# Optimization experiments

Measured on AMD Instinct MI355X. Metric: run time of the kernel, lower is better.

Reference implementation:

```python
import jax, jax.numpy as jnp
import numpy as np

BS, NC, BH, BW, C = 1, 6, 100, 100, 256
HG, WG = 100, 40
HF, WF = 48, 80
HEADS, PTS, HD = 8, 8, 32
MAXOV = 2
NQ = HG * WG


def _nearest_sample(img, grid):
    # img: [B,H,W,Ch], grid: [B,Hg,Wg,2] in [-1,1]; nearest, align_corners=True, zeros padding
    B, H, W, _ = img.shape
    ix = jnp.round((grid[..., 0] + 1.0) * 0.5 * (W - 1))
    iy = jnp.round((grid[..., 1] + 1.0) * 0.5 * (H - 1))
    valid = (ix >= 0) & (ix <= W - 1) & (iy >= 0) & (iy <= H - 1)
    xc = jnp.clip(ix, 0, W - 1).astype(jnp.int32)
    yc = jnp.clip(iy, 0, H - 1).astype(jnp.int32)
    b = jnp.arange(B)[:, None, None]
    return img[b, yc, xc] * valid[..., None]


def _bilinear_sample(img, x, y):
    # img: [B,H,W,Ch]; x,y: [B,N] unnormalized (align_corners=False); zeros padding
    B, H, W, _ = img.shape
    x0 = jnp.floor(x)
    y0 = jnp.floor(y)
    wx1 = x - x0
    wy1 = y - y0
    b = jnp.arange(B)[:, None]

    def corner(xi, yi):
        valid = (xi >= 0) & (xi <= W - 1) & (yi >= 0) & (yi <= H - 1)
        xc = jnp.clip(xi, 0, W - 1).astype(jnp.int32)
        yc = jnp.clip(yi, 0, H - 1).astype(jnp.int32)
        return img[b, yc, xc] * valid[..., None]

    return (corner(x0, y0) * ((1 - wx1) * (1 - wy1))[..., None]
            + corner(x0 + 1, y0) * (wx1 * (1 - wy1))[..., None]
            + corner(x0, y0 + 1) * ((1 - wx1) * wy1)[..., None]
            + corner(x0 + 1, y0 + 1) * (wx1 * wy1)[..., None])


def _forward(query, value, queries_rebatch_grid, restore_bev_grid,
             reference_points_rebatch, bev_pillar_counts, query_pos,
             Wv, bv, Woff, boff, Watt, batt, Wout, bout, spatial_shapes):
    inp_residual = query
    q = query + query_pos                                       # [BS, BH*BW, C]
    # --- rebatch BEV queries per camera via nearest grid_sample ---
    qmap = jnp.broadcast_to(q.reshape(BS, 1, BH, BW, C),
                            (BS, NC, BH, BW, C)).reshape(BS * NC, BH, BW, C)
    q_reb = _nearest_sample(qmap, queries_rebatch_grid).reshape(BS * NC, NQ, C)
    ref = reference_points_rebatch.reshape(BS * NC, NQ, 2)      # flatten(-2): [BNC,NQ,2,1]->[BNC,NQ,2]
    # --- value projection ---
    v = value.transpose(2, 0, 1, 3).reshape(BS * NC, HF * WF, C)
    v = (v @ Wv + bv).reshape(BS * NC, HF, WF, HEADS, HD)
    # --- multi-scale deformable attention (single level) ---
    off = (q_reb @ Woff + boff).reshape(BS * NC, NQ, HEADS, PTS, 2)
    attw = jax.nn.softmax((q_reb @ Watt + batt).reshape(BS * NC, NQ, HEADS, PTS), axis=-1)
    normalizer = jnp.flip(spatial_shapes[0], 0).astype(jnp.float32)  # [WF, HF]
    loc = ref[:, :, None, None, :] + off / normalizer           # [BNC,NQ,HEADS,PTS,2] in [0,1]
    x = (loc[..., 0] * WF - 0.5).transpose(0, 2, 1, 3).reshape(BS * NC * HEADS, NQ * PTS)
    y = (loc[..., 1] * HF - 0.5).transpose(0, 2, 1, 3).reshape(BS * NC * HEADS, NQ * PTS)
    vh = v.transpose(0, 3, 1, 2, 4).reshape(BS * NC * HEADS, HF, WF, HD)
    samp = _bilinear_sample(vh, x, y).reshape(BS * NC, HEADS, NQ, PTS, HD)
    out = jnp.einsum('bhnpd,bnhp->bnhd', samp, attw).reshape(BS * NC, NQ, C)
    queries_out = out.transpose(0, 2, 1)                        # [BNC, C, NQ] (channels-first as module expects)
    # --- restore to BEV feature ---
    qo = queries_out.reshape(BS, NC, C, NQ).transpose(0, 2, 1, 3).reshape(BS, C, NC * HG, WG)
    bevq = _nearest_sample(qo.transpose(0, 2, 3, 1), restore_bev_grid)  # [BS, MAXOV*BH, BW, C]
    bevq = bevq.transpose(0, 3, 1, 2)                           # [BS, C, MAXOV*BH, BW]
    # reshape(BS, C*MAXOV, BH, BW) + all-ones grouped 1x1 conv == sum of the two overlap copies
    slots = bevq[:, :, :BH, :] + bevq[:, :, BH:, :]             # [BS, C, BH, BW]
    slots = slots.reshape(BS, C, BH * BW).transpose(0, 2, 1)    # [BS, BH*BW, C]
    slots = slots * bev_pillar_counts
    slots = slots @ Wout + bout
    return slots + inp_residual  # dropout identity in eval


def setup_inputs():
    key = jax.random.key(0)
    ks = jax.random.split(key, 14)
    s = 1.0 / np.sqrt(C)
    return {
        "query": jax.random.normal(ks[0], (BS, BH * BW, C), jnp.float32),
        "value": jax.random.normal(ks[1], (BS, HF * WF, NC, C), jnp.float32),
        "queries_rebatch_grid": jax.random.uniform(ks[2], (BS * NC, HG, WG, 2), jnp.float32, -1.0, 1.0),
        "restore_bev_grid": jax.random.uniform(ks[3], (BS, MAXOV * BH, BW, 2), jnp.float32, -1.0, 1.0),
        "reference_points_rebatch": jax.random.uniform(ks[4], (BS * NC, NQ, 2, 1), jnp.float32),
        "bev_pillar_counts": jax.random.uniform(ks[5], (BS, BH * BW, 1), jnp.float32),
        "query_pos": jax.random.normal(ks[6], (BS, BH * BW, C), jnp.float32),
        "Wv": jax.random.uniform(ks[7], (C, C), jnp.float32, -s, s),
        "bv": jnp.zeros((C,), jnp.float32),
        "Woff": jax.random.normal(ks[8], (C, HEADS * PTS * 2), jnp.float32) * 0.01,
        "boff": jax.random.uniform(ks[9], (HEADS * PTS * 2,), jnp.float32, -2.0, 2.0),
        "Watt": jax.random.normal(ks[10], (C, HEADS * PTS), jnp.float32) * 0.01,
        "batt": jnp.zeros((HEADS * PTS,), jnp.float32),
        "Wout": jax.random.uniform(ks[11], (C, C), jnp.float32, -s, s),
        "bout": jnp.zeros((C,), jnp.float32),
        "spatial_shapes": jnp.array([[HF, WF]], dtype=jnp.int32),
    }


def reference(query, value, queries_rebatch_grid, restore_bev_grid,
              reference_points_rebatch, bev_pillar_counts, query_pos,
              Wv, bv, Woff, boff, Watt, batt, Wout, bout, spatial_shapes):
    return _forward(query, value, queries_rebatch_grid, restore_bev_grid,
                    reference_points_rebatch, bev_pillar_counts, query_pos,
                    Wv, bv, Woff, boff, Watt, batt, Wout, bout, spatial_shapes)
```

## Files before the change

### kernel.cpp

```cpp
#include <hip/hip_runtime.h>
#include <hip/hip_bf16.h>
#include <math.h>

#define NCAMS 6
#define BH_ 100
#define BW_ 100
#define CDIM 256
#define NQ_ 4000
#define HF_ 48
#define WF_ 80
#define HEADS_ 8
#define PTS_ 8
#define HD_ 32
#define HWV (HF_*WF_)
#define M1_ (NCAMS*HWV)
#define M2_ (NCAMS*NQ_)
#define NOUT_ 10000

#define SA 264
#define SOFF 132
#define SATT 68

typedef __bf16 bf16_t;
typedef __bf16 bf16x8 __attribute__((ext_vector_type(8)));
typedef __bf16 bf16x4 __attribute__((ext_vector_type(4)));
typedef float  f32x4  __attribute__((ext_vector_type(4)));

static __device__ __forceinline__ f32x4 mfma16(bf16x8 a, bf16x8 b, f32x4 c) {
    return __builtin_amdgcn_mfma_f32_16x16x32_bf16(a, b, c, 0, 0, 0);
}

__global__ __launch_bounds__(256) void k0_prep(const float* __restrict__ Wv,
                                               const float* __restrict__ Woff,
                                               const float* __restrict__ Watt,
                                               const float* __restrict__ Wout,
                                               const float* __restrict__ query,
                                               const float* __restrict__ qpos,
                                               bf16_t* __restrict__ WvT,
                                               bf16_t* __restrict__ WcombT,
                                               bf16_t* __restrict__ WoutT,
                                               bf16_t* __restrict__ qsum) {
    int b = blockIdx.x, k = threadIdx.x;
    if (b < 256) {
        WvT[b * 256 + k] = (bf16_t)Wv[k * 256 + b];
    } else if (b < 448) {
        int n = b - 256;
        float v = (n < 128) ? Woff[k * 128 + n] : Watt[k * 64 + (n - 128)];
        WcombT[n * 256 + k] = (bf16_t)v;
    } else if (b < 704) {
        int n = b - 448;
        WoutT[n * 256 + k] = (bf16_t)Wout[k * 256 + n];
    } else {
        int row0 = (b - 704) * 4;
        int r = k >> 6, c4 = k & 63;
        int i = (row0 + r) * 64 + c4;
        float4 a = ((const float4*)query)[i];
        float4 p = ((const float4*)qpos)[i];
        bf16x4 pk;
        pk[0] = (bf16_t)(a.x + p.x); pk[1] = (bf16_t)(a.y + p.y);
        pk[2] = (bf16_t)(a.z + p.z); pk[3] = (bf16_t)(a.w + p.w);
        *(bf16x4*)(qsum + (size_t)i * 4) = pk;
    }
}

__global__ __launch_bounds__(256) void k1_vproj(const float* __restrict__ value,
                                                const bf16_t* __restrict__ WvT,
                                                const float* __restrict__ bv,
                                                bf16_t* __restrict__ vh) {
    __shared__ __align__(16) bf16_t At[32 * SA];
    const int m0 = blockIdx.x * 32;
    const int cam = m0 / HWV;
    const int hw0 = m0 - cam * HWV;
    for (int idx = threadIdx.x; idx < 32 * 64; idx += 256) {
        int r = idx >> 6, c4 = idx & 63;
        float4 v = ((const float4*)value)[((hw0 + r) * NCAMS + cam) * 64 + c4];
        bf16x4 pk; pk[0] = (bf16_t)v.x; pk[1] = (bf16_t)v.y; pk[2] = (bf16_t)v.z; pk[3] = (bf16_t)v.w;
        *(bf16x4*)(At + r * SA + c4 * 4) = pk;
    }
    __syncthreads();
    const int lane = threadIdx.x & 63, w = threadIdx.x >> 6;
    const int lr = lane & 15, lk = lane >> 4;
    f32x4 acc[2][4] = {};
    const bf16_t* a0 = At + lr * SA + lk * 8;
    const bf16_t* b0 = WvT + (w * 64 + lr) * 256 + lk * 8;
#pragma unroll
    for (int ks = 0; ks < 8; ++ks) {
        bf16x8 af[2], bf_[4];
#pragma unroll
        for (int mm = 0; mm < 2; ++mm) af[mm] = *(const bf16x8*)(a0 + mm * 16 * SA + ks * 32);
#pragma unroll
        for (int n = 0; n < 4; ++n) bf_[n] = *(const bf16x8*)(b0 + n * 16 * 256 + ks * 32);
#pragma unroll
        for (int mm = 0; mm < 2; ++mm)
#pragma unroll
            for (int n = 0; n < 4; ++n)
                acc[mm][n] = mfma16(af[mm], bf_[n], acc[mm][n]);
    }
    __syncthreads();
#pragma unroll
    for (int n = 0; n < 4; ++n) {
        int col = w * 64 + n * 16 + lr;
        float bias = bv[col];
#pragma unroll
        for (int mm = 0; mm < 2; ++mm)
#pragma unroll
            for (int j = 0; j < 4; ++j)
                At[(mm * 16 + lk * 4 + j) * SA + col] = (bf16_t)(acc[mm][n][j] + bias);
    }
    __syncthreads();
    for (int idx = threadIdx.x; idx < 32 * 32; idx += 256) {
        int r = idx >> 5, g = idx & 31;
        int head = g >> 2, part = g & 3;
        bf16x8 v = *(const bf16x8*)(At + r * SA + g * 8);
        *(bf16x8*)(vh + ((size_t)(cam * HEADS_ + head) * HWV + hw0 + r) * HD_ + part * 8) = v;
    }
}

__global__ __launch_bounds__(256) void k23_offatt_sample(
        const bf16_t* __restrict__ qsum,
        const float* __restrict__ qgrid,
        const bf16_t* __restrict__ WcombT,
        const float* __restrict__ boff,
        const float* __restrict__ batt,
        const float* __restrict__ refp,
        const bf16_t* __restrict__ vh,
        bf16_t* __restrict__ out_attn) {
    __shared__ __align__(16) char u_lds[16 * SOFF * 4 + 16 * SATT * 4];
    bf16_t* At   = (bf16_t*)u_lds;
    float*  offs = (float*)u_lds;
    float*  atts = (float*)(u_lds + 16 * SOFF * 4);
    __shared__ int rowpos[16];
    __shared__ float rref[16][2];

    const int orig = blockIdx.x;
    const int xcd = orig & 7, idx8 = orig >> 3;
    const int lb = (xcd < 4 ? xcd * 188 : 4 * 188 + (xcd - 4) * 187) + idx8;
    const int m0 = lb * 16;
    const int cam = m0 / NQ_;

    if (threadIdx.x < 16) {
        int m = m0 + threadIdx.x;
        float gx = qgrid[m * 2 + 0], gy = qgrid[m * 2 + 1];
        float fx = rintf(__fmul_rn(__fmul_rn(__fadd_rn(gx, 1.0f), 0.5f), 99.0f));
        float fy = rintf(__fmul_rn(__fmul_rn(__fadd_rn(gy, 1.0f), 0.5f), 99.0f));
        bool valid = (fx >= 0.0f) && (fx <= 99.0f) && (fy >= 0.0f) && (fy <= 99.0f);
        rowpos[threadIdx.x] = valid ? ((int)fy * BW_ + (int)fx) : -1;
    } else if (threadIdx.x < 48) {
        int t = threadIdx.x - 16;
        rref[t >> 1][t & 1] = refp[(m0 + (t >> 1)) * 2 + (t & 1)];
    }
    __syncthreads();
    {
        int idx = threadIdx.x;
#pragma unroll
        for (int it = 0; it < 2; ++it, idx += 256) {
            int r = idx >> 5, g = idx & 31;
            int p = rowpos[r];
            bf16x8 v;
            if (p >= 0) v = *(const bf16x8*)(qsum + (size_t)p * 256 + g * 8);
            else { bf16x8 z = {}; v = z; }
            *(bf16x8*)(At + r * SA + g * 8) = v;
        }
    }
    __syncthreads();
    const int lane = threadIdx.x & 63, w = threadIdx.x >> 6;
    const int lr = lane & 15, lk = lane >> 4;
    const int wcol0 = w * 48;
    f32x4 acc[3] = {};
    {
        const bf16_t* a0 = At + lr * SA + lk * 8;
        const bf16_t* b0 = WcombT + (wcol0 + lr) * 256 + lk * 8;
#pragma unroll
        for (int ks = 0; ks < 8; ++ks) {
            bf16x8 af = *(const bf16x8*)(a0 + ks * 32);
            bf16x8 bf_[3];
#pragma unroll
            for (int n = 0; n < 3; ++n) bf_[n] = *(const bf16x8*)(b0 + n * 16 * 256 + ks * 32);
#pragma unroll
            for (int n = 0; n < 3; ++n)
                acc[n] = mfma16(af, bf_[n], acc[n]);
        }
    }
    __syncthreads();
#pragma unroll
    for (int n = 0; n < 3; ++n) {
        const int colbase = wcol0 + n * 16;
        const int col = colbase + lr;
        const int rloc = lk * 4;
        if (colbase < 128) {
            float bo = boff[col];
#pragma unroll
            for (int j = 0; j < 4; ++j)
                offs[(rloc + j) * SOFF + col] = acc[n][j] + bo;
        } else {
            float bt = batt[col - 128];
#pragma unroll
            for (int j = 0; j < 4; ++j) {
                float lg = acc[n][j] + bt;
                float mx = lg;
                mx = fmaxf(mx, __shfl_xor(mx, 1, 64));
                mx = fmaxf(mx, __shfl_xor(mx, 2, 64));
                mx = fmaxf(mx, __shfl_xor(mx, 4, 64));
                float e = expf(lg - mx);
                float s = e;
                s += __shfl_xor(s, 1, 64);
                s += __shfl_xor(s, 2, 64);
                s += __shfl_xor(s, 4, 64);
                atts[(rloc + j) * SATT + (col - 128)] = e / s;
            }
        }
    }
    __syncthreads();
    const int j = threadIdx.x & 3;
    const int u0 = threadIdx.x >> 2;
    const int r0 = u0 >> 3, h = u0 & 7, r1 = r0 + 8;
    const bf16_t* base = vh + (size_t)(cam * HEADS_ + h) * HWV * HD_ + j * 8;
    const float rxA = rref[r0][0], ryA = rref[r0][1];
    const float rxB = rref[r1][0], ryB = rref[r1][1];
    const float4* offA4 = (const float4*)(offs + r0 * SOFF + h * 16);
    const float4* offB4 = (const float4*)(offs + r1 * SOFF + h * 16);
    float oA[16], oB[16];
#pragma unroll
    for (int q = 0; q < 4; ++q) {
        float4 a = offA4[q], b = offB4[q];
        oA[q * 4 + 0] = a.x; oA[q * 4 + 1] = a.y; oA[q * 4 + 2] = a.z; oA[q * 4 + 3] = a.w;
        oB[q * 4 + 0] = b.x; oB[q * 4 + 1] = b.y; oB[q * 4 + 2] = b.z; oB[q * 4 + 3] = b.w;
    }
    const float* attA = atts + r0 * SATT + h * 8;
    const float* attB = atts + r1 * SATT + h * 8;
    float accA[8] = {}, accB[8] = {};
#pragma unroll
    for (int p = 0; p < PTS_; ++p) {
        float axA = fmaf(rxA, (float)WF_, oA[p * 2 + 0] - 0.5f);
        float ayA = fmaf(ryA, (float)HF_, oA[p * 2 + 1] - 0.5f);
        float xA0f = floorf(axA), yA0f = floorf(ayA);
        float wxA = axA - xA0f, wyA = ayA - yA0f;
        float attA_p = attA[p];
        bool vxA0 = (xA0f >= 0.0f) && (xA0f <= (float)(WF_ - 1));
        bool vxA1 = (xA0f >= -1.0f) && (xA0f <= (float)(WF_ - 2));
        bool vyA0 = (yA0f >= 0.0f) && (yA0f <= (float)(HF_ - 1));
        bool vyA1 = (yA0f >= -1.0f) && (yA0f <= (float)(HF_ - 2));
        float awA00 = (vxA0 && vyA0) ? attA_p * (1.0f - wxA) * (1.0f - wyA) : 0.0f;
        float awA01 = (vxA1 && vyA0) ? attA_p * wxA * (1.0f - wyA) : 0.0f;
        float awA10 = (vxA0 && vyA1) ? attA_p * (1.0f - wxA) * wyA : 0.0f;
        float awA11 = (vxA1 && vyA1) ? attA_p * wxA * wyA : 0.0f;
        int xA0 = (int)fminf(fmaxf(xA0f, 0.0f), (float)(WF_ - 1));
        int xA1 = (int)fminf(fmaxf(xA0f + 1.0f, 0.0f), (float)(WF_ - 1));
        int yA0 = (int)fminf(fmaxf(yA0f, 0.0f), (float)(HF_ - 1));
        int yA1 = (int)fminf(fmaxf(yA0f + 1.0f, 0.0f), (float)(HF_ - 1));
        float axB = fmaf(rxB, (float)WF_, oB[p * 2 + 0] - 0.5f);
        float ayB = fmaf(ryB, (float)HF_, oB[p * 2 + 1] - 0.5f);
        float xB0f = floorf(axB), yB0f = floorf(ayB);
        float wxB = axB - xB0f, wyB = ayB - yB0f;
        float attB_p = attB[p];
        bool vxB0 = (xB0f >= 0.0f) && (xB0f <= (float)(WF_ - 1));
        bool vxB1 = (xB0f >= -1.0f) && (xB0f <= (float)(WF_ - 2));
        bool vyB0 = (yB0f >= 0.0f) && (yB0f <= (float)(HF_ - 1));
        bool vyB1 = (yB0f >= -1.0f) && (yB0f <= (float)(HF_ - 2));
        float awB00 = (vxB0 && vyB0) ? attB_p * (1.0f - wxB) * (1.0f - wyB) : 0.0f;
        float awB01 = (vxB1 && vyB0) ? attB_p * wxB * (1.0f - wyB) : 0.0f;
        float awB10 = (vxB0 && vyB1) ? attB_p * (1.0f - wxB) * wyB : 0.0f;
        float awB11 = (vxB1 && vyB1) ? attB_p * wxB * wyB : 0.0f;
        int xB0 = (int)fminf(fmaxf(xB0f, 0.0f), (float)(WF_ - 1));
        int xB1 = (int)fminf(fmaxf(xB0f + 1.0f, 0.0f), (float)(WF_ - 1));
        int yB0 = (int)fminf(fmaxf(yB0f, 0.0f), (float)(HF_ - 1));
        int yB1 = (int)fminf(fmaxf(yB0f + 1.0f, 0.0f), (float)(HF_ - 1));
        bf16x8 cA00 = *(const bf16x8*)(base + (yA0 * WF_ + xA0) * HD_);
        bf16x8 cA01 = *(const bf16x8*)(base + (yA0 * WF_ + xA1) * HD_);
        bf16x8 cA10 = *(const bf16x8*)(base + (yA1 * WF_ + xA0) * HD_);
        bf16x8 cA11 = *(const bf16x8*)(base + (yA1 * WF_ + xA1) * HD_);
        bf16x8 cB00 = *(const bf16x8*)(base + (yB0 * WF_ + xB0) * HD_);
        bf16x8 cB01 = *(const bf16x8*)(base + (yB0 * WF_ + xB1) * HD_);
        bf16x8 cB10 = *(const bf16x8*)(base + (yB1 * WF_ + xB0) * HD_);
        bf16x8 cB11 = *(const bf16x8*)(base + (yB1 * WF_ + xB1) * HD_);
#pragma unroll
        for (int c = 0; c < 8; ++c) {
            accA[c] = fmaf(awA00, (float)cA00[c],
                      fmaf(awA01, (float)cA01[c],
                      fmaf(awA10, (float)cA10[c],
                      fmaf(awA11, (float)cA11[c], accA[c]))));
            accB[c] = fmaf(awB00, (float)cB00[c],
                      fmaf(awB01, (float)cB01[c],
                      fmaf(awB10, (float)cB10[c],
                      fmaf(awB11, (float)cB11[c], accB[c]))));
        }
    }
    bf16x8 ovA, ovB;
#pragma unroll
    for (int c = 0; c < 8; ++c) { ovA[c] = (bf16_t)accA[c]; ovB[c] = (bf16_t)accB[c]; }
    *(bf16x8*)(out_attn + (size_t)(m0 + r0) * CDIM + h * HD_ + j * 8) = ovA;
    *(bf16x8*)(out_attn + (size_t)(m0 + r1) * CDIM + h * HD_ + j * 8) = ovB;
}

__global__ __launch_bounds__(256) void k4_restore(const bf16_t* __restrict__ out_attn,
                                                  const float* __restrict__ rgrid,
                                                  const float* __restrict__ counts,
                                                  const bf16_t* __restrict__ WoutT,
                                                  const float* __restrict__ bout,
                                                  const float* __restrict__ query,
                                                  float* __restrict__ out) {
    __shared__ __align__(16) bf16_t At[32 * SA];
    __shared__ int pos2[32][2];
    __shared__ float cnt[32];
    const int m0 = blockIdx.x * 32;
    if (threadIdx.x < 64) {
        int r = threadIdx.x >> 1, k = threadIdx.x & 1;
        int i = m0 + r;
        if (i < NOUT_) {
            int bh = i / 100, bw = i - bh * 100;
            int R = bh + k * BH_;
            float gx = rgrid[(R * 100 + bw) * 2 + 0], gy = rgrid[(R * 100 + bw) * 2 + 1];
            float fx = rintf(__fmul_rn(__fmul_rn(__fadd_rn(gx, 1.0f), 0.5f), 39.0f));
            float fy = rintf(__fmul_rn(__fmul_rn(__fadd_rn(gy, 1.0f), 0.5f), 599.0f));
            bool valid = (fx >= 0.0f) && (fx <= 39.0f) && (fy >= 0.0f) && (fy <= 599.0f);
            int ix = (int)fx, iy = (int)fy;
            int camr = iy / 100, hg = iy - camr * 100;
            pos2[r][k] = valid ? (camr * NQ_ + hg * 40 + ix) : -1;
            if (k == 0) cnt[r] = counts[i];
        } else {
            pos2[r][k] = -1;
            if (k == 0) cnt[r] = 0.0f;
        }
    }
    __syncthreads();
    for (int idx = threadIdx.x; idx < 32 * 32; idx += 256) {
        int r = idx >> 5, g = idx & 31;
        int p0 = pos2[r][0], p1 = pos2[r][1];
        float s[8] = {};
        if (p0 >= 0) {
            bf16x8 a = *(const bf16x8*)(out_attn + (size_t)p0 * CDIM + g * 8);
#pragma unroll
            for (int c = 0; c < 8; ++c) s[c] += (float)a[c];
        }
        if (p1 >= 0) {
            bf16x8 a = *(const bf16x8*)(out_attn + (size_t)p1 * CDIM + g * 8);
#pragma unroll
            for (int c = 0; c < 8; ++c) s[c] += (float)a[c];
        }
        float cn = cnt[r];
        bf16x8 pk;
#pragma unroll
        for (int c = 0; c < 8; ++c) pk[c] = (bf16_t)(s[c] * cn);
        *(bf16x8*)(At + r * SA + g * 8) = pk;
    }
    __syncthreads();
    const int lane = threadIdx.x & 63, w = threadIdx.x >> 6;
    const int lr = lane & 15, lk = lane >> 4;
    f32x4 acc[2][4] = {};
    const bf16_t* a0 = At + lr * SA + lk * 8;
    const bf16_t* b0 = WoutT + (w * 64 + lr) * 256 + lk * 8;
#pragma unroll
    for (int ks = 0; ks < 8; ++ks) {
        bf16x8 af[2], bf_[4];
#pragma unroll
        for (int mm = 0; mm < 2; ++mm) af[mm] = *(const bf16x8*)(a0 + mm * 16 * SA + ks * 32);
#pragma unroll
        for (int n = 0; n < 4; ++n) bf_[n] = *(const bf16x8*)(b0 + n * 16 * 256 + ks * 32);
#pragma unroll
        for (int mm = 0; mm < 2; ++mm)
#pragma unroll
            for (int n = 0; n < 4; ++n)
                acc[mm][n] = mfma16(af[mm], bf_[n], acc[mm][n]);
    }
#pragma unroll
    for (int n = 0; n < 4; ++n) {
        int col = w * 64 + n * 16 + lr;
        float bo = bout[col];
#pragma unroll
        for (int mm = 0; mm < 2; ++mm)
#pragma unroll
            for (int j = 0; j < 4; ++j) {
                int row = m0 + mm * 16 + lk * 4 + j;
                if (row < NOUT_)
                    out[row * CDIM + col] = acc[mm][n][j] + bo + query[row * CDIM + col];
            }
    }
}

extern "C" void kernel_launch(void* const* d_in, const int* in_sizes, int n_in,
                              void* d_out, int out_size, void* d_ws, size_t ws_size,
                              hipStream_t stream) {
    (void)in_sizes; (void)n_in; (void)out_size; (void)ws_size;
    const float* query  = (const float*)d_in[0];
    const float* value  = (const float*)d_in[1];
    const float* qgrid  = (const float*)d_in[2];
    const float* rgrid  = (const float*)d_in[3];
    const float* refp   = (const float*)d_in[4];
    const float* counts = (const float*)d_in[5];
    const float* qpos   = (const float*)d_in[6];
    const float* Wv     = (const float*)d_in[7];
    const float* bv     = (const float*)d_in[8];
    const float* Woff   = (const float*)d_in[9];
    const float* boff   = (const float*)d_in[10];
    const float* Watt   = (const float*)d_in[11];
    const float* batt   = (const float*)d_in[12];
    const float* Wout   = (const float*)d_in[13];
    const float* bout   = (const float*)d_in[14];
    float* out = (float*)d_out;
    char* w8 = (char*)d_ws;

    bf16_t* vh       = (bf16_t*)(w8);
    bf16_t* out_attn = (bf16_t*)(w8 + 11796480);
    bf16_t* WvT      = (bf16_t*)(w8 + 24084480);
    bf16_t* WcombT   = (bf16_t*)(w8 + 24215552);
    bf16_t* WoutT    = (bf16_t*)(w8 + 24313856);
    bf16_t* qsum     = (bf16_t*)(w8 + 24444928);

    hipLaunchKernelGGL(k0_prep,   dim3(3204),     dim3(256), 0, stream, Wv, Woff, Watt, Wout,
                       query, qpos, WvT, WcombT, WoutT, qsum);
    hipLaunchKernelGGL(k1_vproj,  dim3(M1_ / 32), dim3(256), 0, stream, value, WvT, bv, vh);
    hipLaunchKernelGGL(k23_offatt_sample, dim3(M2_ / 16), dim3(256), 0, stream,
                       qsum, qgrid, WcombT, boff, batt, refp, vh, out_attn);
    hipLaunchKernelGGL(k4_restore, dim3(313),     dim3(256), 0, stream, out_attn, rgrid, counts,
                       WoutT, bout, query, out);
}
```

Baseline: 94.45 us.

## Sort rebatched queries into spatial bins by reference point before sampling

Adds a counting sort (count, scan, scatter kernels) that groups the camera queries by a 20x12 spatial bin of their reference point. The fused offset/attention/sampling kernel then processes queries in that permuted order, reading per-row camera and writing output at the original row index. The goal is better cache locality for the bilinear value gathers. In exchange it adds three small kernel launches and atomics, and uses an indirect gather of query rows. Scatter order within a bin is nondeterministic, but the output stays correct.

```diff
diff --git a/kernel.cpp b/kernel.cpp
--- a/kernel.cpp
+++ b/kernel.cpp
@@ -16,6 +16,7 @@
 #define M1_ (NCAMS*HWV)
 #define M2_ (NCAMS*NQ_)
 #define NOUT_ 10000
+#define NBINS 1440
 
 #define SA 264
 #define SOFF 132
@@ -39,7 +40,8 @@
                                                bf16_t* __restrict__ WvT,
                                                bf16_t* __restrict__ WcombT,
                                                bf16_t* __restrict__ WoutT,
-                                               bf16_t* __restrict__ qsum) {
+                                               bf16_t* __restrict__ qsum,
+                                               int* __restrict__ bin_cnt) {
     int b = blockIdx.x, k = threadIdx.x;
     if (b < 256) {
         WvT[b * 256 + k] = (bf16_t)Wv[k * 256 + b];
@@ -50,7 +52,7 @@
     } else if (b < 704) {
         int n = b - 448;
         WoutT[n * 256 + k] = (bf16_t)Wout[k * 256 + n];
-    } else {
+    } else if (b < 3204) {
         int row0 = (b - 704) * 4;
         int r = k >> 6, c4 = k & 63;
         int i = (row0 + r) * 64 + c4;
@@ -60,7 +62,60 @@
         pk[0] = (bf16_t)(a.x + p.x); pk[1] = (bf16_t)(a.y + p.y);
         pk[2] = (bf16_t)(a.z + p.z); pk[3] = (bf16_t)(a.w + p.w);
         *(bf16x4*)(qsum + (size_t)i * 4) = pk;
-    }
+    } else {
+        int idx = (b - 3204) * 256 + k;
+        if (idx < NBINS) bin_cnt[idx] = 0;
+    }
+}
+
+__global__ __launch_bounds__(256) void kb_count(const float* __restrict__ refp,
+                                                int* __restrict__ bin_of_m,
+                                                int* __restrict__ bin_cnt) {
+    int m = blockIdx.x * 256 + threadIdx.x;
+    if (m >= M2_) return;
+    float rx = refp[m * 2 + 0], ry = refp[m * 2 + 1];
+    int cam = m / NQ_;
+    int tx = min(max((int)(rx * 20.0f), 0), 19);
+    int ty = min(max((int)(ry * 12.0f), 0), 11);
+    int bin = cam * 240 + ty * 20 + tx;
+    bin_of_m[m] = bin;
+    atomicAdd(&bin_cnt[bin], 1);
+}
+
+__global__ __launch_bounds__(256) void kb_scan(const int* __restrict__ bin_cnt,
+                                               int* __restrict__ bin_off) {
+    __shared__ int part[240];
+    int t = threadIdx.x;
+    if (t < 240) {
+        int s = 0;
+#pragma unroll
+        for (int i = 0; i < 6; ++i) s += bin_cnt[t * 6 + i];
+        part[t] = s;
+    }
+    __syncthreads();
+    if (t == 0) {
+        int run = 0;
+        for (int i = 0; i < 240; ++i) { int v = part[i]; part[i] = run; run += v; }
+    }
+    __syncthreads();
+    if (t < 240) {
+        int run = part[t];
+#pragma unroll
+        for (int i = 0; i < 6; ++i) {
+            int bidx = t * 6 + i;
+            bin_off[bidx] = run;
+            run += bin_cnt[bidx];
+        }
+    }
+}
+
+__global__ __launch_bounds__(256) void kb_scatter(const int* __restrict__ bin_of_m,
+                                                  int* __restrict__ bin_off,
+                                                  int* __restrict__ perm) {
+    int m = blockIdx.x * 256 + threadIdx.x;
+    if (m >= M2_) return;
+    int pos = atomicAdd(&bin_off[bin_of_m[m]], 1);
+    perm[pos] = m;
 }
 
 __global__ __launch_bounds__(256) void k1_vproj(const float* __restrict__ value,
@@ -117,6 +172,7 @@
 }
 
 __global__ __launch_bounds__(256) void k23_offatt_sample(
+        const int* __restrict__ perm,
         const bf16_t* __restrict__ qsum,
         const float* __restrict__ qgrid,
         const bf16_t* __restrict__ WcombT,
@@ -129,6 +185,8 @@
     bf16_t* At   = (bf16_t*)u_lds;
     float*  offs = (float*)u_lds;
     float*  atts = (float*)(u_lds + 16 * SOFF * 4);
+    __shared__ int mlist[16];
+    __shared__ int rcam[16];
     __shared__ int rowpos[16];
     __shared__ float rref[16][2];
 
@@ -136,18 +194,19 @@
     const int xcd = orig & 7, idx8 = orig >> 3;
     const int lb = (xcd < 4 ? xcd * 188 : 4 * 188 + (xcd - 4) * 187) + idx8;
     const int m0 = lb * 16;
-    const int cam = m0 / NQ_;
 
     if (threadIdx.x < 16) {
-        int m = m0 + threadIdx.x;
+        int r = threadIdx.x;
+        int m = perm[m0 + r];
+        mlist[r] = m;
+        rcam[r] = m / NQ_;
         float gx = qgrid[m * 2 + 0], gy = qgrid[m * 2 + 1];
         float fx = rintf(__fmul_rn(__fmul_rn(__fadd_rn(gx, 1.0f), 0.5f), 99.0f));
         float fy = rintf(__fmul_rn(__fmul_rn(__fadd_rn(gy, 1.0f), 0.5f), 99.0f));
         bool valid = (fx >= 0.0f) && (fx <= 99.0f) && (fy >= 0.0f) && (fy <= 99.0f);
-        rowpos[threadIdx.x] = valid ? ((int)fy * BW_ + (int)fx) : -1;
-    } else if (threadIdx.x < 48) {
-        int t = threadIdx.x - 16;
-        rref[t >> 1][t & 1] = refp[(m0 + (t >> 1)) * 2 + (t & 1)];
+        rowpos[r] = valid ? ((int)fy * BW_ + (int)fx) : -1;
+        rref[r][0] = refp[m * 2 + 0];
+        rref[r][1] = refp[m * 2 + 1];
     }
     __syncthreads();
     {
@@ -214,7 +273,8 @@
     const int j = threadIdx.x & 3;
     const int u0 = threadIdx.x >> 2;
     const int r0 = u0 >> 3, h = u0 & 7, r1 = r0 + 8;
-    const bf16_t* base = vh + (size_t)(cam * HEADS_ + h) * HWV * HD_ + j * 8;
+    const bf16_t* baseA = vh + (size_t)(rcam[r0] * HEADS_ + h) * HWV * HD_ + j * 8;
+    const bf16_t* baseB = vh + (size_t)(rcam[r1] * HEADS_ + h) * HWV * HD_ + j * 8;
     const float rxA = rref[r0][0], ryA = rref[r0][1];
     const float rxB = rref[r1][0], ryB = rref[r1][1];
     const float4* offA4 = (const float4*)(offs + r0 * SOFF + h * 16);
@@ -265,14 +325,14 @@
         int xB1 = (int)fminf(fmaxf(xB0f + 1.0f, 0.0f), (float)(WF_ - 1));
         int yB0 = (int)fminf(fmaxf(yB0f, 0.0f), (float)(HF_ - 1));
         int yB1 = (int)fminf(fmaxf(yB0f + 1.0f, 0.0f), (float)(HF_ - 1));
-        bf16x8 cA00 = *(const bf16x8*)(base + (yA0 * WF_ + xA0) * HD_);
-        bf16x8 cA01 = *(const bf16x8*)(base + (yA0 * WF_ + xA1) * HD_);
-        bf16x8 cA10 = *(const bf16x8*)(base + (yA1 * WF_ + xA0) * HD_);
-        bf16x8 cA11 = *(const bf16x8*)(base + (yA1 * WF_ + xA1) * HD_);
-        bf16x8 cB00 = *(const bf16x8*)(base + (yB0 * WF_ + xB0) * HD_);
-        bf16x8 cB01 = *(const bf16x8*)(base + (yB0 * WF_ + xB1) * HD_);
-        bf16x8 cB10 = *(const bf16x8*)(base + (yB1 * WF_ + xB0) * HD_);
-        bf16x8 cB11 = *(const bf16x8*)(base + (yB1 * WF_ + xB1) * HD_);
+        bf16x8 cA00 = *(const bf16x8*)(baseA + (yA0 * WF_ + xA0) * HD_);
+        bf16x8 cA01 = *(const bf16x8*)(baseA + (yA0 * WF_ + xA1) * HD_);
+        bf16x8 cA10 = *(const bf16x8*)(baseA + (yA1 * WF_ + xA0) * HD_);
+        bf16x8 cA11 = *(const bf16x8*)(baseA + (yA1 * WF_ + xA1) * HD_);
+        bf16x8 cB00 = *(const bf16x8*)(baseB + (yB0 * WF_ + xB0) * HD_);
+        bf16x8 cB01 = *(const bf16x8*)(baseB + (yB0 * WF_ + xB1) * HD_);
+        bf16x8 cB10 = *(const bf16x8*)(baseB + (yB1 * WF_ + xB0) * HD_);
+        bf16x8 cB11 = *(const bf16x8*)(baseB + (yB1 * WF_ + xB1) * HD_);
 #pragma unroll
         for (int c = 0; c < 8; ++c) {
             accA[c] = fmaf(awA00, (float)cA00[c],
@@ -288,8 +348,8 @@
     bf16x8 ovA, ovB;
 #pragma unroll
     for (int c = 0; c < 8; ++c) { ovA[c] = (bf16_t)accA[c]; ovB[c] = (bf16_t)accB[c]; }
-    *(bf16x8*)(out_attn + (size_t)(m0 + r0) * CDIM + h * HD_ + j * 8) = ovA;
-    *(bf16x8*)(out_attn + (size_t)(m0 + r1) * CDIM + h * HD_ + j * 8) = ovB;
+    *(bf16x8*)(out_attn + (size_t)mlist[r0] * CDIM + h * HD_ + j * 8) = ovA;
+    *(bf16x8*)(out_attn + (size_t)mlist[r1] * CDIM + h * HD_ + j * 8) = ovB;
 }
 
 __global__ __launch_bounds__(256) void k4_restore(const bf16_t* __restrict__ out_attn,
@@ -405,12 +465,19 @@
     bf16_t* WcombT   = (bf16_t*)(w8 + 24215552);
     bf16_t* WoutT    = (bf16_t*)(w8 + 24313856);
     bf16_t* qsum     = (bf16_t*)(w8 + 24444928);
-
-    hipLaunchKernelGGL(k0_prep,   dim3(3204),     dim3(256), 0, stream, Wv, Woff, Watt, Wout,
-                       query, qpos, WvT, WcombT, WoutT, qsum);
+    int* bin_cnt     = (int*)(w8 + 29564928);
+    int* bin_off     = (int*)(w8 + 29570688);
+    int* bin_of_m    = (int*)(w8 + 29576448);
+    int* perm        = (int*)(w8 + 29672448);
+
+    hipLaunchKernelGGL(k0_prep,   dim3(3210),     dim3(256), 0, stream, Wv, Woff, Watt, Wout,
+                       query, qpos, WvT, WcombT, WoutT, qsum, bin_cnt);
+    hipLaunchKernelGGL(kb_count,  dim3(94),       dim3(256), 0, stream, refp, bin_of_m, bin_cnt);
+    hipLaunchKernelGGL(kb_scan,   dim3(1),        dim3(256), 0, stream, bin_cnt, bin_off);
+    hipLaunchKernelGGL(kb_scatter, dim3(94),      dim3(256), 0, stream, bin_of_m, bin_off, perm);
     hipLaunchKernelGGL(k1_vproj,  dim3(M1_ / 32), dim3(256), 0, stream, value, WvT, bv, vh);
     hipLaunchKernelGGL(k23_offatt_sample, dim3(M2_ / 16), dim3(256), 0, stream,
-                       qsum, qgrid, WcombT, boff, batt, refp, vh, out_attn);
+                       perm, qsum, qgrid, WcombT, boff, batt, refp, vh, out_attn);
     hipLaunchKernelGGL(k4_restore, dim3(313),     dim3(256), 0, stream, out_attn, rgrid, counts,
                        WoutT, bout, query, out);
 }
```

After: 103.7 us. 9.8% more time.

## Store a one-column-shifted copy of value map so bilinear pairs align

Applied to the files above, without the earlier changes.

The value projection kernel now writes a second copy of the per-head value map shifted by one x column. The sampler picks the copy by the parity of the left x index, so each bilinear x-pair starts at an even column and sits in one aligned 128-byte span. Boundary handling is moved into weight remapping. This is meant to cut cache-line and sector splits in the gather loads, at the cost of doubling the value-map writes and workspace.

```diff
diff --git a/kernel.cpp b/kernel.cpp
--- a/kernel.cpp
+++ b/kernel.cpp
@@ -16,6 +16,7 @@
 #define M1_ (NCAMS*HWV)
 #define M2_ (NCAMS*NQ_)
 #define NOUT_ 10000
+#define VHSHIFT 5898240
 
 #define SA 264
 #define SOFF 132
@@ -112,7 +113,14 @@
         int r = idx >> 5, g = idx & 31;
         int head = g >> 2, part = g & 3;
         bf16x8 v = *(const bf16x8*)(At + r * SA + g * 8);
-        *(bf16x8*)(vh + ((size_t)(cam * HEADS_ + head) * HWV + hw0 + r) * HD_ + part * 8) = v;
+        int hw = hw0 + r;
+        int y = hw / WF_;
+        int x = hw - y * WF_;
+        size_t rowbase = ((size_t)(cam * HEADS_ + head) * HF_ + y) * (WF_ * HD_);
+        int o = x * HD_ + part * 8;
+        *(bf16x8*)(vh + rowbase + o) = v;
+        if (o >= 32) *(bf16x8*)(vh + VHSHIFT + rowbase + o - 32) = v;
+        if (x == WF_ - 1) *(bf16x8*)(vh + VHSHIFT + rowbase + o) = v;
     }
 }
 
@@ -244,10 +252,17 @@
         float awA01 = (vxA1 && vyA0) ? attA_p * wxA * (1.0f - wyA) : 0.0f;
         float awA10 = (vxA0 && vyA1) ? attA_p * (1.0f - wxA) * wyA : 0.0f;
         float awA11 = (vxA1 && vyA1) ? attA_p * wxA * wyA : 0.0f;
-        int xA0 = (int)fminf(fmaxf(xA0f, 0.0f), (float)(WF_ - 1));
-        int xA1 = (int)fminf(fmaxf(xA0f + 1.0f, 0.0f), (float)(WF_ - 1));
+        bool pxA = (xA0f >= 0.0f);
+        float wA00 = pxA ? awA00 : awA01;
+        float wA01 = pxA ? awA01 : 0.0f;
+        float wA10 = pxA ? awA10 : awA11;
+        float wA11 = pxA ? awA11 : 0.0f;
+        int xsA = (int)fminf(fmaxf(xA0f, 0.0f), (float)(WF_ - 1));
+        int parA = xsA & 1;
+        int tbA = xsA - parA;
         int yA0 = (int)fminf(fmaxf(yA0f, 0.0f), (float)(HF_ - 1));
         int yA1 = (int)fminf(fmaxf(yA0f + 1.0f, 0.0f), (float)(HF_ - 1));
+        const bf16_t* bpA = base + (size_t)parA * VHSHIFT;
         float axB = fmaf(rxB, (float)WF_, oB[p * 2 + 0] - 0.5f);
         float ayB = fmaf(ryB, (float)HF_, oB[p * 2 + 1] - 0.5f);
         float xB0f = floorf(axB), yB0f = floorf(ayB);
@@ -261,28 +276,35 @@
         float awB01 = (vxB1 && vyB0) ? attB_p * wxB * (1.0f - wyB) : 0.0f;
         float awB10 = (vxB0 && vyB1) ? attB_p * (1.0f - wxB) * wyB : 0.0f;
         float awB11 = (vxB1 && vyB1) ? attB_p * wxB * wyB : 0.0f;
-        int xB0 = (int)fminf(fmaxf(xB0f, 0.0f), (float)(WF_ - 1));
-        int xB1 = (int)fminf(fmaxf(xB0f + 1.0f, 0.0f), (float)(WF_ - 1));
+        bool pxB = (xB0f >= 0.0f);
+        float wB00 = pxB ? awB00 : awB01;
+        float wB01 = pxB ? awB01 : 0.0f;
+        float wB10 = pxB ? awB10 : awB11;
+        float wB11 = pxB ? awB11 : 0.0f;
+        int xsB = (int)fminf(fmaxf(xB0f, 0.0f), (float)(WF_ - 1));
+        int parB = xsB & 1;
+        int tbB = xsB - parB;
         int yB0 = (int)fminf(fmaxf(yB0f, 0.0f), (float)(HF_ - 1));
         int yB1 = (int)fminf(fmaxf(yB0f + 1.0f, 0.0f), (float)(HF_ - 1));
-        bf16x8 cA00 = *(const bf16x8*)(base + (yA0 * WF_ + xA0) * HD_);
-        bf16x8 cA01 = *(const bf16x8*)(base + (yA0 * WF_ + xA1) * HD_);
-        bf16x8 cA10 = *(const bf16x8*)(base + (yA1 * WF_ + xA0) * HD_);
-        bf16x8 cA11 = *(const bf16x8*)(base + (yA1 * WF_ + xA1) * HD_);
-        bf16x8 cB00 = *(const bf16x8*)(base + (yB0 * WF_ + xB0) * HD_);
-        bf16x8 cB01 = *(const bf16x8*)(base + (yB0 * WF_ + xB1) * HD_);
-        bf16x8 cB10 = *(const bf16x8*)(base + (yB1 * WF_ + xB0) * HD_);
-        bf16x8 cB11 = *(const bf16x8*)(base + (yB1 * WF_ + xB1) * HD_);
+        const bf16_t* bpB = base + (size_t)parB * VHSHIFT;
+        bf16x8 eA00 = *(const bf16x8*)(bpA + (yA0 * WF_ + tbA) * HD_);
+        bf16x8 eA01 = *(const bf16x8*)(bpA + (yA0 * WF_ + tbA + 1) * HD_);
+        bf16x8 eA10 = *(const bf16x8*)(bpA + (yA1 * WF_ + tbA) * HD_);
+        bf16x8 eA11 = *(const bf16x8*)(bpA + (yA1 * WF_ + tbA + 1) * HD_);
+        bf16x8 eB00 = *(const bf16x8*)(bpB + (yB0 * WF_ + tbB) * HD_);
+        bf16x8 eB01 = *(const bf16x8*)(bpB + (yB0 * WF_ + tbB + 1) * HD_);
+        bf16x8 eB10 = *(const bf16x8*)(bpB + (yB1 * WF_ + tbB) * HD_);
+        bf16x8 eB11 = *(const bf16x8*)(bpB + (yB1 * WF_ + tbB + 1) * HD_);
 #pragma unroll
         for (int c = 0; c < 8; ++c) {
-            accA[c] = fmaf(awA00, (float)cA00[c],
-                      fmaf(awA01, (float)cA01[c],
-                      fmaf(awA10, (float)cA10[c],
-                      fmaf(awA11, (float)cA11[c], accA[c]))));
-            accB[c] = fmaf(awB00, (float)cB00[c],
-                      fmaf(awB01, (float)cB01[c],
-                      fmaf(awB10, (float)cB10[c],
-                      fmaf(awB11, (float)cB11[c], accB[c]))));
+            accA[c] = fmaf(wA00, (float)eA00[c],
+                      fmaf(wA01, (float)eA01[c],
+                      fmaf(wA10, (float)eA10[c],
+                      fmaf(wA11, (float)eA11[c], accA[c]))));
+            accB[c] = fmaf(wB00, (float)eB00[c],
+                      fmaf(wB01, (float)eB01[c],
+                      fmaf(wB10, (float)eB10[c],
+                      fmaf(wB11, (float)eB11[c], accB[c]))));
         }
     }
     bf16x8 ovA, ovB;
@@ -400,11 +422,11 @@
     char* w8 = (char*)d_ws;
 
     bf16_t* vh       = (bf16_t*)(w8);
-    bf16_t* out_attn = (bf16_t*)(w8 + 11796480);
-    bf16_t* WvT      = (bf16_t*)(w8 + 24084480);
-    bf16_t* WcombT   = (bf16_t*)(w8 + 24215552);
-    bf16_t* WoutT    = (bf16_t*)(w8 + 24313856);
-    bf16_t* qsum     = (bf16_t*)(w8 + 24444928);
+    bf16_t* out_attn = (bf16_t*)(w8 + 23592960);
+    bf16_t* WvT      = (bf16_t*)(w8 + 35880960);
+    bf16_t* WcombT   = (bf16_t*)(w8 + 36012032);
+    bf16_t* WoutT    = (bf16_t*)(w8 + 36110336);
+    bf16_t* qsum     = (bf16_t*)(w8 + 36241408);
 
     hipLaunchKernelGGL(k0_prep,   dim3(3204),     dim3(256), 0, stream, Wv, Woff, Watt, Wout,
                        query, qpos, WvT, WcombT, WoutT, qsum);
```

Result: slower. 97.23 us (+2.9%).

## Store projected value in fp8 with paired-column copies for wider gathers

Applied to the files above, without the earlier changes.

The value projection now writes its output as fp8 (e4m3 via cvt_pk_fp8) rather than bf16. It also writes a second copy shifted by one column, so each 32-byte x-pair of corners can be fetched with one 16-byte load per lane. The sampler now loads two rows per point instead of four corners, converts fp8 to f32, and merges the x-halves with a lane shuffle. This is meant to halve gather bytes and cut the number of scattered loads. In exchange it loses precision in the sampled values and adds duplicate writes plus extra shuffles.

```diff
diff --git a/kernel.cpp b/kernel.cpp
--- a/kernel.cpp
+++ b/kernel.cpp
@@ -16,6 +16,7 @@
 #define M1_ (NCAMS*HWV)
 #define M2_ (NCAMS*NQ_)
 #define NOUT_ 10000
+#define VHBYTES 5898240
 
 #define SA 264
 #define SOFF 132
@@ -25,6 +26,7 @@
 typedef __bf16 bf16x8 __attribute__((ext_vector_type(8)));
 typedef __bf16 bf16x4 __attribute__((ext_vector_type(4)));
 typedef float  f32x4  __attribute__((ext_vector_type(4)));
+typedef float  f32x2  __attribute__((ext_vector_type(2)));
 
 static __device__ __forceinline__ f32x4 mfma16(bf16x8 a, bf16x8 b, f32x4 c) {
     return __builtin_amdgcn_mfma_f32_16x16x32_bf16(a, b, c, 0, 0, 0);
@@ -66,7 +68,7 @@
 __global__ __launch_bounds__(256) void k1_vproj(const float* __restrict__ value,
                                                 const bf16_t* __restrict__ WvT,
                                                 const float* __restrict__ bv,
-                                                bf16_t* __restrict__ vh) {
+                                                unsigned char* __restrict__ vh8) {
     __shared__ __align__(16) bf16_t At[32 * SA];
     const int m0 = blockIdx.x * 32;
     const int cam = m0 / HWV;
@@ -112,7 +114,20 @@
         int r = idx >> 5, g = idx & 31;
         int head = g >> 2, part = g & 3;
         bf16x8 v = *(const bf16x8*)(At + r * SA + g * 8);
-        *(bf16x8*)(vh + ((size_t)(cam * HEADS_ + head) * HWV + hw0 + r) * HD_ + part * 8) = v;
+        int d0 = 0, d1 = 0;
+        d0 = __builtin_amdgcn_cvt_pk_fp8_f32((float)v[0], (float)v[1], d0, false);
+        d0 = __builtin_amdgcn_cvt_pk_fp8_f32((float)v[2], (float)v[3], d0, true);
+        d1 = __builtin_amdgcn_cvt_pk_fp8_f32((float)v[4], (float)v[5], d1, false);
+        d1 = __builtin_amdgcn_cvt_pk_fp8_f32((float)v[6], (float)v[7], d1, true);
+        int2 pk8 = make_int2(d0, d1);
+        int hw = hw0 + r;
+        int y = hw / WF_;
+        int x = hw - y * WF_;
+        size_t rowbase = (size_t)(cam * HEADS_ + head) * 122880 + (size_t)y * (WF_ * 32);
+        int o = x * 32 + part * 8;
+        *(int2*)(vh8 + rowbase + o) = pk8;
+        if (o >= 32) *(int2*)(vh8 + VHBYTES + rowbase + o - 32) = pk8;
+        if (x == WF_ - 1) *(int2*)(vh8 + VHBYTES + rowbase + o) = pk8;
     }
 }
 
@@ -123,7 +138,7 @@
         const float* __restrict__ boff,
         const float* __restrict__ batt,
         const float* __restrict__ refp,
-        const bf16_t* __restrict__ vh,
+        const unsigned char* __restrict__ vh8,
         bf16_t* __restrict__ out_attn) {
     __shared__ __align__(16) char u_lds[16 * SOFF * 4 + 16 * SATT * 4];
     bf16_t* At   = (bf16_t*)u_lds;
@@ -211,10 +226,12 @@
         }
     }
     __syncthreads();
-    const int j = threadIdx.x & 3;
+    const int chh  = threadIdx.x & 1;
+    const int xsel = (threadIdx.x >> 1) & 1;
+    const int lanoff = (threadIdx.x & 3) * 16;
     const int u0 = threadIdx.x >> 2;
     const int r0 = u0 >> 3, h = u0 & 7, r1 = r0 + 8;
-    const bf16_t* base = vh + (size_t)(cam * HEADS_ + h) * HWV * HD_ + j * 8;
+    const unsigned char* bslice = vh8 + (size_t)(cam * HEADS_ + h) * 122880;
     const float rxA = rref[r0][0], ryA = rref[r0][1];
     const float rxB = rref[r1][0], ryB = rref[r1][1];
     const float4* offA4 = (const float4*)(offs + r0 * SOFF + h * 16);
@@ -228,7 +245,7 @@
     }
     const float* attA = atts + r0 * SATT + h * 8;
     const float* attB = atts + r1 * SATT + h * 8;
-    float accA[8] = {}, accB[8] = {};
+    float accA[16] = {}, accB[16] = {};
 #pragma unroll
     for (int p = 0; p < PTS_; ++p) {
         float axA = fmaf(rxA, (float)WF_, oA[p * 2 + 0] - 0.5f);
@@ -244,10 +261,15 @@
         float awA01 = (vxA1 && vyA0) ? attA_p * wxA * (1.0f - wyA) : 0.0f;
         float awA10 = (vxA0 && vyA1) ? attA_p * (1.0f - wxA) * wyA : 0.0f;
         float awA11 = (vxA1 && vyA1) ? attA_p * wxA * wyA : 0.0f;
-        int xA0 = (int)fminf(fmaxf(xA0f, 0.0f), (float)(WF_ - 1));
-        int xA1 = (int)fminf(fmaxf(xA0f + 1.0f, 0.0f), (float)(WF_ - 1));
+        bool pxA = (xA0f >= 0.0f);
+        float wqA0 = xsel ? (pxA ? awA01 : 0.0f) : (pxA ? awA00 : awA01);
+        float wqA1 = xsel ? (pxA ? awA11 : 0.0f) : (pxA ? awA10 : awA11);
+        int xsA = (int)fminf(fmaxf(xA0f, 0.0f), (float)(WF_ - 1));
+        int parA = xsA & 1;
+        int tbA = xsA - parA;
         int yA0 = (int)fminf(fmaxf(yA0f, 0.0f), (float)(HF_ - 1));
         int yA1 = (int)fminf(fmaxf(yA0f + 1.0f, 0.0f), (float)(HF_ - 1));
+        const unsigned char* bpA = bslice + (size_t)parA * VHBYTES;
         float axB = fmaf(rxB, (float)WF_, oB[p * 2 + 0] - 0.5f);
         float ayB = fmaf(ryB, (float)HF_, oB[p * 2 + 1] - 0.5f);
         float xB0f = floorf(axB), yB0f = floorf(ayB);
@@ -261,35 +283,69 @@
         float awB01 = (vxB1 && vyB0) ? attB_p * wxB * (1.0f - wyB) : 0.0f;
         float awB10 = (vxB0 && vyB1) ? attB_p * (1.0f - wxB) * wyB : 0.0f;
         float awB11 = (vxB1 && vyB1) ? attB_p * wxB * wyB : 0.0f;
-        int xB0 = (int)fminf(fmaxf(xB0f, 0.0f), (float)(WF_ - 1));
-        int xB1 = (int)fminf(fmaxf(xB0f + 1.0f, 0.0f), (float)(WF_ - 1));
+        bool pxB = (xB0f >= 0.0f);
+        float wqB0 = xsel ? (pxB ? awB01 : 0.0f) : (pxB ? awB00 : awB01);
+        float wqB1 = xsel ? (pxB ? awB11 : 0.0f) : (pxB ? awB10 : awB11);
+        int xsB = (int)fminf(fmaxf(xB0f, 0.0f), (float)(WF_ - 1));
+        int parB = xsB & 1;
+        int tbB = xsB - parB;
         int yB0 = (int)fminf(fmaxf(yB0f, 0.0f), (float)(HF_ - 1));
         int yB1 = (int)fminf(fmaxf(yB0f + 1.0f, 0.0f), (float)(HF_ - 1));
-        bf16x8 cA00 = *(const bf16x8*)(base + (yA0 * WF_ + xA0) * HD_);
-        bf16x8 cA01 = *(const bf16x8*)(base + (yA0 * WF_ + xA1) * HD_);
-        bf16x8 cA10 = *(const bf16x8*)(base + (yA1 * WF_ + xA0) * HD_);
-        bf16x8 cA11 = *(const bf16x8*)(base + (yA1 * WF_ + xA1) * HD_);
-        bf16x8 cB00 = *(const bf16x8*)(base + (yB0 * WF_ + xB0) * HD_);
-        bf16x8 cB01 = *(const bf16x8*)(base + (yB0 * WF_ + xB1) * HD_);
-        bf16x8 cB10 = *(const bf16x8*)(base + (yB1 * WF_ + xB0) * HD_);
-        bf16x8 cB11 = *(const bf16x8*)(base + (yB1 * WF_ + xB1) * HD_);
+        const unsigned char* bpB = bslice + (size_t)parB * VHBYTES;
+        int4 qA0 = *(const int4*)(bpA + (yA0 * WF_ + tbA) * 32 + lanoff);
+        int4 qA1 = *(const int4*)(bpA + (yA1 * WF_ + tbA) * 32 + lanoff);
+        int4 qB0 = *(const int4*)(bpB + (yB0 * WF_ + tbB) * 32 + lanoff);
+        int4 qB1 = *(const int4*)(bpB + (yB1 * WF_ + tbB) * 32 + lanoff);
+        int dA0[4] = {qA0.x, qA0.y, qA0.z, qA0.w};
+        int dA1[4] = {qA1.x, qA1.y, qA1.z, qA1.w};
+        int dB0[4] = {qB0.x, qB0.y, qB0.z, qB0.w};
+        int dB1[4] = {qB1.x, qB1.y, qB1.z, qB1.w};
+#pragma unroll
+        for (int kq = 0; kq < 4; ++kq) {
+            f32x2 lo, hi;
+            lo = __builtin_amdgcn_cvt_pk_f32_fp8(dA0[kq], false);
+            hi = __builtin_amdgcn_cvt_pk_f32_fp8(dA0[kq], true);
+            accA[kq * 4 + 0] = fmaf(wqA0, lo[0], accA[kq * 4 + 0]);
+            accA[kq * 4 + 1] = fmaf(wqA0, lo[1], accA[kq * 4 + 1]);
+            accA[kq * 4 + 2] = fmaf(wqA0, hi[0], accA[kq * 4 + 2]);
+            accA[kq * 4 + 3] = fmaf(wqA0, hi[1], accA[kq * 4 + 3]);
+            lo = __builtin_amdgcn_cvt_pk_f32_fp8(dA1[kq], false);
+            hi = __builtin_amdgcn_cvt_pk_f32_fp8(dA1[kq], true);
+            accA[kq * 4 + 0] = fmaf(wqA1, lo[0], accA[kq * 4 + 0]);
+            accA[kq * 4 + 1] = fmaf(wqA1, lo[1], accA[kq * 4 + 1]);
+            accA[kq * 4 + 2] = fmaf(wqA1, hi[0], accA[kq * 4 + 2]);
+            accA[kq * 4 + 3] = fmaf(wqA1, hi[1], accA[kq * 4 + 3]);
+            lo = __builtin_amdgcn_cvt_pk_f32_fp8(dB0[kq], false);
+            hi = __builtin_amdgcn_cvt_pk_f32_fp8(dB0[kq], true);
+            accB[kq * 4 + 0] = fmaf(wqB0, lo[0], accB[kq * 4 + 0]);
+            accB[kq * 4 + 1] = fmaf(wqB0, lo[1], accB[kq * 4 + 1]);
+            accB[kq * 4 + 2] = fmaf(wqB0, hi[0], accB[kq * 4 + 2]);
+            accB[kq * 4 + 3] = fmaf(wqB0, hi[1], accB[kq * 4 + 3]);
+            lo = __builtin_amdgcn_cvt_pk_f32_fp8(dB1[kq], false);
+            hi = __builtin_amdgcn_cvt_pk_f32_fp8(dB1[kq], true);
+            accB[kq * 4 + 0] = fmaf(wqB1, lo[0], accB[kq * 4 + 0]);
+            accB[kq * 4 + 1] = fmaf(wqB1, lo[1], accB[kq * 4 + 1]);
+            accB[kq * 4 + 2] = fmaf(wqB1, hi[0], accB[kq * 4 + 2]);
+            accB[kq * 4 + 3] = fmaf(wqB1, hi[1], accB[kq * 4 + 3]);
+        }
+    }
+#pragma unroll
+    for (int c = 0; c < 16; ++c) {
+        accA[c] += __shfl_xor(accA[c], 2, 64);
+        accB[c] += __shfl_xor(accB[c], 2, 64);
+    }
+    if (xsel == 0) {
+        bf16x8 a0v, a1v, b0v, b1v;
 #pragma unroll
         for (int c = 0; c < 8; ++c) {
-            accA[c] = fmaf(awA00, (float)cA00[c],
-                      fmaf(awA01, (float)cA01[c],
-                      fmaf(awA10, (float)cA10[c],
-                      fmaf(awA11, (float)cA11[c], accA[c]))));
-            accB[c] = fmaf(awB00, (float)cB00[c],
-                      fmaf(awB01, (float)cB01[c],
-                      fmaf(awB10, (float)cB10[c],
-                      fmaf(awB11, (float)cB11[c], accB[c]))));
-        }
-    }
-    bf16x8 ovA, ovB;
-#pragma unroll
-    for (int c = 0; c < 8; ++c) { ovA[c] = (bf16_t)accA[c]; ovB[c] = (bf16_t)accB[c]; }
-    *(bf16x8*)(out_attn + (size_t)(m0 + r0) * CDIM + h * HD_ + j * 8) = ovA;
-    *(bf16x8*)(out_attn + (size_t)(m0 + r1) * CDIM + h * HD_ + j * 8) = ovB;
+            a0v[c] = (bf16_t)accA[c]; a1v[c] = (bf16_t)accA[c + 8];
+            b0v[c] = (bf16_t)accB[c]; b1v[c] = (bf16_t)accB[c + 8];
+        }
+        bf16_t* dA = out_attn + (size_t)(m0 + r0) * CDIM + h * HD_ + chh * 16;
+        bf16_t* dB = out_attn + (size_t)(m0 + r1) * CDIM + h * HD_ + chh * 16;
+        *(bf16x8*)(dA) = a0v; *(bf16x8*)(dA + 8) = a1v;
+        *(bf16x8*)(dB) = b0v; *(bf16x8*)(dB + 8) = b1v;
+    }
 }
 
 __global__ __launch_bounds__(256) void k4_restore(const bf16_t* __restrict__ out_attn,
@@ -399,7 +455,7 @@
     float* out = (float*)d_out;
     char* w8 = (char*)d_ws;
 
-    bf16_t* vh       = (bf16_t*)(w8);
+    unsigned char* vh8 = (unsigned char*)(w8);
     bf16_t* out_attn = (bf16_t*)(w8 + 11796480);
     bf16_t* WvT      = (bf16_t*)(w8 + 24084480);
     bf16_t* WcombT   = (bf16_t*)(w8 + 24215552);
@@ -408,9 +464,9 @@
 
     hipLaunchKernelGGL(k0_prep,   dim3(3204),     dim3(256), 0, stream, Wv, Woff, Watt, Wout,
                        query, qpos, WvT, WcombT, WoutT, qsum);
-    hipLaunchKernelGGL(k1_vproj,  dim3(M1_ / 32), dim3(256), 0, stream, value, WvT, bv, vh);
+    hipLaunchKernelGGL(k1_vproj,  dim3(M1_ / 32), dim3(256), 0, stream, value, WvT, bv, vh8);
     hipLaunchKernelGGL(k23_offatt_sample, dim3(M2_ / 16), dim3(256), 0, stream,
-                       qsum, qgrid, WcombT, boff, batt, refp, vh, out_attn);
+                       qsum, qgrid, WcombT, boff, batt, refp, vh8, out_attn);
     hipLaunchKernelGGL(k4_restore, dim3(313),     dim3(256), 0, stream, out_attn, rgrid, counts,
                        WoutT, bout, query, out);
 }
```

Result: faster. 90.55 us, median of 2 (-4.1%).
